# Optimization experiments

Measured on AMD Instinct MI355X. Metric: run time of the kernel, lower is better.

The kernel has to match this reference:

```python
import jax, jax.numpy as jnp
import numpy as np
from jax import lax

STRIDE = 1
PADDING = 3


def setup_inputs() -> dict:
    key = jax.random.key(0)
    k1, k2 = jax.random.split(key)
    X = jax.random.normal(k1, (64, 1024, 1024), dtype=jnp.float32)
    W = jax.random.normal(k2, (7, 7), dtype=jnp.float32)
    return {"X": X, "W": W}


def reference(X, W):
    # Single-channel batched 2D cross-correlation with stride + symmetric padding.
    # X: [B, M, N] -> lhs [B, 1, M, N]; W: [u, v] -> rhs [1, 1, u, v]
    out = lax.conv_general_dilated(
        X[:, None, :, :],
        W[None, None, :, :],
        window_strides=(STRIDE, STRIDE),
        padding=[(PADDING, PADDING), (PADDING, PADDING)],
        dimension_numbers=("NCHW", "OIHW", "NCHW"),
    )
    return out[:, 0, :, :]  # [B, out_h, out_w]
```

## Files before the change

kernel.cpp:

```cpp
#include <hip/hip_runtime.h>

#define IN_H   1024
#define IN_W   1024
#define TILE_X 128
#define TILE_Y 32
#define LDS_H  38
#define LDS_W  136
#define ROW_F4 34

__global__ __launch_bounds__(256)
void conv7x7_kernel(const float* __restrict__ X,
                    const float* __restrict__ W,
                    float* __restrict__ out) {
    __shared__ float lds[LDS_H * LDS_W];

    const int tid = threadIdx.x;
    const int x0  = blockIdx.x * TILE_X;
    const int y0  = blockIdx.y * TILE_Y;
    const int b   = blockIdx.z;

    const float* Ximg = X + (size_t)b * IN_H * IN_W;

    const int gx = x0 - 4;
    const int gy = y0 - 3;

    const bool interior = (gx >= 0) && (gx + LDS_W <= IN_W) &&
                          (gy >= 0) && (gy + LDS_H <= IN_H);

    if (interior) {
        for (int i = tid; i < LDS_H * ROW_F4; i += 256) {
            int r = i / ROW_F4;
            int c = i - r * ROW_F4;
            float4 v = *(const float4*)(Ximg + (gy + r) * IN_W + gx + c * 4);
            *(float4*)&lds[r * LDS_W + c * 4] = v;
        }
    } else {
        for (int i = tid; i < LDS_H * ROW_F4; i += 256) {
            int r   = i / ROW_F4;
            int c   = i - r * ROW_F4;
            int row = gy + r;
            float4 v = make_float4(0.f, 0.f, 0.f, 0.f);
            if (row >= 0 && row < IN_H) {
                const float* p = Ximg + row * IN_W;
                int col = gx + c * 4;
                v.x = (col + 0 >= 0 && col + 0 < IN_W) ? p[col + 0] : 0.f;
                v.y = (col + 1 >= 0 && col + 1 < IN_W) ? p[col + 1] : 0.f;
                v.z = (col + 2 >= 0 && col + 2 < IN_W) ? p[col + 2] : 0.f;
                v.w = (col + 3 >= 0 && col + 3 < IN_W) ? p[col + 3] : 0.f;
            }
            *(float4*)&lds[r * LDS_W + c * 4] = v;
        }
    }

    float w[49];
    #pragma unroll
    for (int k = 0; k < 49; ++k) w[k] = W[k];

    __syncthreads();

    const int tx  = tid & 31;
    const int tyq = tid >> 5;

    float acc[4][4];
    #pragma unroll
    for (int o = 0; o < 4; ++o)
        #pragma unroll
        for (int c = 0; c < 4; ++c) acc[o][c] = 0.f;

    const int base_col = tx * 4;

    #pragma unroll
    for (int r = 0; r < 10; ++r) {
        const float* row = &lds[(tyq * 4 + r) * LDS_W + base_col];
        float4 a = *(const float4*)(row);
        float4 bq = *(const float4*)(row + 4);
        float4 cq = *(const float4*)(row + 8);
        float s[12] = { a.x, a.y, a.z, a.w,
                        bq.x, bq.y, bq.z, bq.w,
                        cq.x, cq.y, cq.z, cq.w };
        #pragma unroll
        for (int o = 0; o < 4; ++o) {
            const int ky = r - o;
            if (ky >= 0 && ky < 7) {
                #pragma unroll
                for (int kx = 0; kx < 7; ++kx) {
                    const float wv = w[ky * 7 + kx];
                    #pragma unroll
                    for (int c = 0; c < 4; ++c)
                        acc[o][c] += wv * s[1 + c + kx];
                }
            }
        }
    }

    float* Oimg = out + (size_t)b * IN_H * IN_W;
    const int ox = x0 + tx * 4;
    #pragma unroll
    for (int o = 0; o < 4; ++o) {
        const int oy = y0 + tyq * 4 + o;
        float4 v = make_float4(acc[o][0], acc[o][1], acc[o][2], acc[o][3]);
        *(float4*)(Oimg + (size_t)oy * IN_W + ox) = v;
    }
}

extern "C" void kernel_launch(void* const* d_in, const int* in_sizes, int n_in,
                              void* d_out, int out_size, void* d_ws, size_t ws_size,
                              hipStream_t stream) {
    const float* X = (const float*)d_in[0];
    const float* W = (const float*)d_in[1];
    float* out = (float*)d_out;

    dim3 grid(IN_W / TILE_X, IN_H / TILE_Y, 64);
    conv7x7_kernel<<<grid, 256, 0, stream>>>(X, W, out);
}
```

Measured before the change: 461.5 us.

## Double output rows per thread, enlarge tile to 64 rows, use nontemporal stores

Each thread now computes 8 output rows instead of 4, and the tile height doubles to 64. This reduces the halo overhead per tile (70 rows loaded for 64 produced versus 38 for 32) and the LDS row reads per output (14 reads for 8 rows versus 10 for 4). Output stores become nontemporal so results skip cache retention. Launch bounds now request 4 blocks per CU. The larger accumulator raises register pressure, and the LDS footprint roughly doubles, which may reduce occupancy.

```diff
diff --git a/kernel.cpp b/kernel.cpp
--- a/kernel.cpp
+++ b/kernel.cpp
@@ -3,16 +3,19 @@
 #define IN_H   1024
 #define IN_W   1024
 #define TILE_X 128
-#define TILE_Y 32
-#define LDS_H  38
+#define TILE_Y 64
+#define LDS_H  70
 #define LDS_W  136
 #define ROW_F4 34
+#define STAGE_N (LDS_H * ROW_F4)
 
-__global__ __launch_bounds__(256)
+typedef float vfloat4 __attribute__((ext_vector_type(4)));
+
+__global__ __launch_bounds__(256, 4)
 void conv7x7_kernel(const float* __restrict__ X,
                     const float* __restrict__ W,
                     float* __restrict__ out) {
-    __shared__ float lds[LDS_H * LDS_W];
+    __shared__ __align__(16) float lds[LDS_H * LDS_W];
 
     const int tid = threadIdx.x;
     const int x0  = blockIdx.x * TILE_X;
@@ -28,27 +31,27 @@
                           (gy >= 0) && (gy + LDS_H <= IN_H);
 
     if (interior) {
-        for (int i = tid; i < LDS_H * ROW_F4; i += 256) {
-            int r = i / ROW_F4;
-            int c = i - r * ROW_F4;
-            float4 v = *(const float4*)(Ximg + (gy + r) * IN_W + gx + c * 4);
-            *(float4*)&lds[r * LDS_W + c * 4] = v;
+        for (int idx = tid; idx < STAGE_N; idx += 256) {
+            int r = idx / ROW_F4;
+            int c = idx - r * ROW_F4;
+            vfloat4 v = *(const vfloat4*)(Ximg + (size_t)(gy + r) * IN_W + gx + c * 4);
+            *(vfloat4*)&lds[r * LDS_W + c * 4] = v;
         }
     } else {
-        for (int i = tid; i < LDS_H * ROW_F4; i += 256) {
-            int r   = i / ROW_F4;
-            int c   = i - r * ROW_F4;
+        for (int idx = tid; idx < STAGE_N; idx += 256) {
+            int r   = idx / ROW_F4;
+            int c   = idx - r * ROW_F4;
             int row = gy + r;
-            float4 v = make_float4(0.f, 0.f, 0.f, 0.f);
+            vfloat4 v = {0.f, 0.f, 0.f, 0.f};
             if (row >= 0 && row < IN_H) {
-                const float* p = Ximg + row * IN_W;
+                const float* p = Ximg + (size_t)row * IN_W;
                 int col = gx + c * 4;
                 v.x = (col + 0 >= 0 && col + 0 < IN_W) ? p[col + 0] : 0.f;
                 v.y = (col + 1 >= 0 && col + 1 < IN_W) ? p[col + 1] : 0.f;
                 v.z = (col + 2 >= 0 && col + 2 < IN_W) ? p[col + 2] : 0.f;
                 v.w = (col + 3 >= 0 && col + 3 < IN_W) ? p[col + 3] : 0.f;
             }
-            *(float4*)&lds[r * LDS_W + c * 4] = v;
+            *(vfloat4*)&lds[r * LDS_W + c * 4] = v;
         }
     }
 
@@ -58,28 +61,29 @@
 
     __syncthreads();
 
-    const int tx  = tid & 31;
-    const int tyq = tid >> 5;
+    const int tx = tid & 31;
+    const int ty = tid >> 5;
 
-    float acc[4][4];
+    float acc[8][4];
     #pragma unroll
-    for (int o = 0; o < 4; ++o)
+    for (int o = 0; o < 8; ++o)
         #pragma unroll
         for (int c = 0; c < 4; ++c) acc[o][c] = 0.f;
 
     const int base_col = tx * 4;
 
     #pragma unroll
-    for (int r = 0; r < 10; ++r) {
-        const float* row = &lds[(tyq * 4 + r) * LDS_W + base_col];
-        float4 a = *(const float4*)(row);
-        float4 bq = *(const float4*)(row + 4);
-        float4 cq = *(const float4*)(row + 8);
-        float s[12] = { a.x, a.y, a.z, a.w,
-                        bq.x, bq.y, bq.z, bq.w,
-                        cq.x, cq.y, cq.z, cq.w };
+    for (int r = 0; r < 14; ++r) {
+        const float* row = &lds[(ty * 8 + r) * LDS_W + base_col];
+        vfloat4 A = *(const vfloat4*)(row);
+        vfloat4 B = *(const vfloat4*)(row + 4);
+        vfloat4 C = *(const vfloat4*)(row + 8);
+        asm volatile("" : "+v"(A), "+v"(B), "+v"(C));
+        float s[12] = { A.x, A.y, A.z, A.w,
+                        B.x, B.y, B.z, B.w,
+                        C.x, C.y, C.z, C.w };
         #pragma unroll
-        for (int o = 0; o < 4; ++o) {
+        for (int o = 0; o < 8; ++o) {
             const int ky = r - o;
             if (ky >= 0 && ky < 7) {
                 #pragma unroll
@@ -96,10 +100,10 @@
     float* Oimg = out + (size_t)b * IN_H * IN_W;
     const int ox = x0 + tx * 4;
     #pragma unroll
-    for (int o = 0; o < 4; ++o) {
-        const int oy = y0 + tyq * 4 + o;
-        float4 v = make_float4(acc[o][0], acc[o][1], acc[o][2], acc[o][3]);
-        *(float4*)(Oimg + (size_t)oy * IN_W + ox) = v;
+    for (int o = 0; o < 8; ++o) {
+        const int oy = y0 + ty * 8 + o;
+        vfloat4 v = { acc[o][0], acc[o][1], acc[o][2], acc[o][3] };
+        __builtin_nontemporal_store(v, (vfloat4*)(Oimg + (size_t)oy * IN_W + ox));
     }
 }
 
```

After: 1.129 ms. +144.6%, slower.
